# Kernel optimization log

Hardware: AMD Instinct MI355X
Metric: run time of the kernel (lower is better)

The kernel has to match this reference:

```python
import jax, jax.numpy as jnp
import numpy as np

B, T, D, L = 64, 512, 768, 50


def setup_inputs() -> dict:
    key = jax.random.key(0)
    ks = jax.random.split(key, 8)
    input_emb = jax.random.normal(ks[0], (B, T, D), jnp.float32)
    labels = jax.random.randint(ks[1], (B, T), 0, L, jnp.int32)
    # contiguous valid-prefix mask (torchcrf requires mask[:,0]=1)
    lengths = jax.random.randint(ks[2], (B,), T // 2, T + 1)
    label_mask = jnp.arange(T)[None, :] < lengths[:, None]  # bool [B,T]
    W = jax.random.normal(ks[3], (D, L), jnp.float32) * (1.0 / np.sqrt(D))
    b = jnp.zeros((L,), jnp.float32)
    start_transitions = jax.random.uniform(ks[4], (L,), jnp.float32, -0.1, 0.1)
    end_transitions = jax.random.uniform(ks[5], (L,), jnp.float32, -0.1, 0.1)
    transitions = jax.random.uniform(ks[6], (L, L), jnp.float32, -0.1, 0.1)
    return {"input_emb": input_emb, "labels": labels, "label_mask": label_mask,
            "W": W, "b": b, "start_transitions": start_transitions,
            "end_transitions": end_transitions, "transitions": transitions}


def _crf_llh(logits, labels, mask, start_t, end_t, trans):
    """torchcrf log-likelihood, batch_first inputs -> [B] llh."""
    em = jnp.transpose(logits, (1, 0, 2))        # [T,B,L] time-major
    tags = jnp.transpose(labels)                 # [T,B]
    m = jnp.transpose(mask).astype(logits.dtype)  # [T,B]
    bidx = jnp.arange(logits.shape[0])

    # --- numerator: score of gold path ---
    score0 = start_t[tags[0]] + em[0, bidx, tags[0]]

    def num_step(carry, x):
        score, prev = carry
        em_t, tag_t, m_t = x
        step = trans[prev, tag_t] + em_t[bidx, tag_t]
        score = score + step * m_t
        prev = jnp.where(m_t > 0, tag_t, prev)  # track last valid tag
        return (score, prev), None

    (num, last_tags), _ = jax.lax.scan(num_step, (score0, tags[0]),
                                       (em[1:], tags[1:], m[1:]))
    num = num + end_t[last_tags]

    # --- denominator: forward algorithm ---
    alpha0 = start_t[None, :] + em[0]  # [B,L]

    def den_step(alpha, x):
        em_t, m_t = x
        nxt = jax.nn.logsumexp(alpha[:, :, None] + trans[None, :, :], axis=1) + em_t
        return jnp.where(m_t[:, None] > 0, nxt, alpha), None

    alpha, _ = jax.lax.scan(den_step, alpha0, (em[1:], m[1:]))
    den = jax.nn.logsumexp(alpha + end_t[None, :], axis=1)
    return num - den


def reference(input_emb, labels, label_mask, W, b, start_transitions,
              end_transitions, transitions):
    # dropout is identity in eval mode
    logits = input_emb @ W + b  # [B,T,L]
    llh = _crf_llh(logits, labels, label_mask, start_transitions,
                   end_transitions, transitions)
    loss = llh.mean()  # reduction='mean' over batch
    return (-loss, logits)
```

## Files before the change

### kernel.cpp

```cpp
#include <hip/hip_runtime.h>
#include <hip/hip_bf16.h>
#include <math.h>

#define BATCH 64
#define TLEN 512
#define DIM 768
#define NLAB 50

typedef __attribute__((ext_vector_type(8))) short short8;
typedef __attribute__((ext_vector_type(4))) float f32x4;

__device__ __forceinline__ unsigned short f2bf(float f) {
    unsigned int u = __float_as_uint(f);
    return (unsigned short)((u + 0x7FFFu + ((u >> 16) & 1u)) >> 16);
}

__global__ __launch_bounds__(256) void wprep_kernel(const float* __restrict__ W,
                                                    unsigned short* __restrict__ Bt) {
    int idx = blockIdx.x * 256 + threadIdx.x;
    if (idx < 64 * DIM) {
        int c = idx / DIM;
        int k = idx - c * DIM;
        float v = (c < NLAB) ? W[k * NLAB + c] : 0.f;
        Bt[idx] = f2bf(v);
    }
}

#define AST 36
#define BSTC 40

__global__ __launch_bounds__(512)
void gemm_kernel(
    const float* __restrict__ A,
    const unsigned short* __restrict__ Bt,
    const float* __restrict__ bias,
    float* __restrict__ out)
{
    __shared__ float As[2][128 * AST];
    __shared__ short Bs[2][64 * BSTC];

    const int tid = threadIdx.x;
    const int wave = tid >> 6;
    const int lane = tid & 63;
    const int m = lane & 15;
    const int q = lane >> 4;
    const int row0 = blockIdx.x * 128;

    const int r0s = tid >> 2;
    const int c0s = (tid & 3) * 8;
    const int bcol = tid >> 3;
    const int bkk = (tid & 7) * 4;

    f32x4 acc0 = {0.f,0.f,0.f,0.f}, acc1 = {0.f,0.f,0.f,0.f};
    f32x4 acc2 = {0.f,0.f,0.f,0.f}, acc3 = {0.f,0.f,0.f,0.f};

    {
        *(float4*)&As[0][r0s * AST + c0s]     = *(const float4*)(A + (size_t)(row0 + r0s) * DIM + c0s);
        *(float4*)&As[0][r0s * AST + c0s + 4] = *(const float4*)(A + (size_t)(row0 + r0s) * DIM + c0s + 4);
        *(short4*)&Bs[0][bcol * BSTC + bkk]   = *(const short4*)(Bt + (size_t)bcol * DIM + bkk);
    }
    __syncthreads();

    int buf = 0;
    for (int ch = 0; ch < DIM / 32; ++ch) {
        const int k0n = (ch + 1) * 32;
        const bool havenext = (ch < DIM / 32 - 1);
        float4 pa0, pa1;
        short4 pb;
        if (havenext) {
            pa0 = *(const float4*)(A + (size_t)(row0 + r0s) * DIM + k0n + c0s);
            pa1 = *(const float4*)(A + (size_t)(row0 + r0s) * DIM + k0n + c0s + 4);
            pb  = *(const short4*)(Bt + (size_t)bcol * DIM + k0n + bkk);
        }

        const short8 bq0 = *(const short8*)&Bs[buf][( 0 + m) * BSTC + q * 8];
        const short8 bq1 = *(const short8*)&Bs[buf][(16 + m) * BSTC + q * 8];
        const short8 bq2 = *(const short8*)&Bs[buf][(32 + m) * BSTC + q * 8];
        const short8 bq3 = *(const short8*)&Bs[buf][(48 + m) * BSTC + q * 8];

        {
            const int rr = wave * 16 + m;
            const float4 xa = *(const float4*)&As[buf][rr * AST + q * 8];
            const float4 xb = *(const float4*)&As[buf][rr * AST + q * 8 + 4];
            short8 af;
            af[0] = (short)f2bf(xa.x); af[1] = (short)f2bf(xa.y);
            af[2] = (short)f2bf(xa.z); af[3] = (short)f2bf(xa.w);
            af[4] = (short)f2bf(xb.x); af[5] = (short)f2bf(xb.y);
            af[6] = (short)f2bf(xb.z); af[7] = (short)f2bf(xb.w);
            acc0 = __builtin_amdgcn_mfma_f32_16x16x32_bf16(af, bq0, acc0, 0, 0, 0);
            acc1 = __builtin_amdgcn_mfma_f32_16x16x32_bf16(af, bq1, acc1, 0, 0, 0);
            acc2 = __builtin_amdgcn_mfma_f32_16x16x32_bf16(af, bq2, acc2, 0, 0, 0);
            acc3 = __builtin_amdgcn_mfma_f32_16x16x32_bf16(af, bq3, acc3, 0, 0, 0);
        }

        if (havenext) {
            const int nb = buf ^ 1;
            *(float4*)&As[nb][r0s * AST + c0s]     = pa0;
            *(float4*)&As[nb][r0s * AST + c0s + 4] = pa1;
            *(short4*)&Bs[nb][bcol * BSTC + bkk]   = pb;
        }
        __syncthreads();
        buf ^= 1;
    }

    const int rb = row0 + wave * 16 + q * 4;
#pragma unroll
    for (int nt = 0; nt < 4; ++nt) {
        const f32x4 av = (nt == 0) ? acc0 : (nt == 1) ? acc1 : (nt == 2) ? acc2 : acc3;
        const int col = nt * 16 + m;
        if (col < NLAB) {
            const float bv = bias[col];
#pragma unroll
            for (int r = 0; r < 4; ++r)
                out[(size_t)(rb + r) * NLAB + col] = av[r] + bv;
        }
    }
}

__device__ __forceinline__ float wave_sum(float v) {
#pragma unroll
    for (int off = 32; off > 0; off >>= 1) v += __shfl_xor(v, off, 64);
    return v;
}

#define ET_INIT(v, base)                            \
    v.x = __expf(trans[(base + 0) * NLAB + j]);     \
    v.y = __expf(trans[(base + 1) * NLAB + j]);     \
    v.z = __expf(trans[(base + 2) * NLAB + j]);     \
    v.w = __expf(trans[(base + 3) * NLAB + j]);

#define RLF(i) __uint_as_float(__builtin_amdgcn_readlane(__float_as_uint(ue), (i)))

__global__ __launch_bounds__(64) __attribute__((amdgpu_waves_per_eu(1, 1)))
void crf_kernel(
    const float* __restrict__ logits,
    const int* __restrict__ labels,
    const void* __restrict__ maskp,
    const float* __restrict__ startT,
    const float* __restrict__ endT,
    const float* __restrict__ trans,
    float* __restrict__ llh) {
    const int b = blockIdx.x;
    const int lane = threadIdx.x;

    const int probe = ((const int*)maskp)[0];
    int len = 0;
    if (probe == 1) {
        const int* mk = (const int*)maskp + b * TLEN;
#pragma unroll
        for (int it = 0; it < 8; ++it)
            len += (int)__popcll(__ballot(mk[lane + it * 64] != 0));
    } else if (probe == 0x01010101) {
        const unsigned char* mk = (const unsigned char*)maskp + b * TLEN;
#pragma unroll
        for (int it = 0; it < 8; ++it)
            len += (int)__popcll(__ballot(mk[lane + it * 64] != 0));
    } else if (probe == 0x3F803F80) {
        const unsigned short* mk = (const unsigned short*)maskp + b * TLEN;
#pragma unroll
        for (int it = 0; it < 8; ++it)
            len += (int)__popcll(__ballot(mk[lane + it * 64] != 0));
    } else {
        const float* mk = (const float*)maskp + b * TLEN;
#pragma unroll
        for (int it = 0; it < 8; ++it)
            len += (int)__popcll(__ballot(mk[lane + it * 64] != 0.f));
    }

    const int j = lane;
    const int jc = (j < NLAB) ? j : (NLAB - 1);

    float4 et0  = {0.f,0.f,0.f,0.f}, et1  = {0.f,0.f,0.f,0.f};
    float4 et2  = {0.f,0.f,0.f,0.f}, et3  = {0.f,0.f,0.f,0.f};
    float4 et4  = {0.f,0.f,0.f,0.f}, et5  = {0.f,0.f,0.f,0.f};
    float4 et6  = {0.f,0.f,0.f,0.f}, et7  = {0.f,0.f,0.f,0.f};
    float4 et8  = {0.f,0.f,0.f,0.f}, et9  = {0.f,0.f,0.f,0.f};
    float4 et10 = {0.f,0.f,0.f,0.f}, et11 = {0.f,0.f,0.f,0.f};
    float4 et12 = {0.f,0.f,0.f,0.f};
    if (j < NLAB) {
        ET_INIT(et0,  0)  ET_INIT(et1,  4)  ET_INIT(et2,  8)
        ET_INIT(et3,  12) ET_INIT(et4,  16) ET_INIT(et5,  20)
        ET_INIT(et6,  24) ET_INIT(et7,  28) ET_INIT(et8,  32)
        ET_INIT(et9,  36) ET_INIT(et10, 40) ET_INIT(et11, 44)
        et12.x = __expf(trans[48 * NLAB + j]);
        et12.y = __expf(trans[49 * NLAB + j]);
    }

    const float* em = logits + (size_t)b * TLEN * NLAB;

    float a0v = (j < NLAB) ? (startT[j] + em[j]) : 0.f;
    const float Abc = __shfl(a0v, 0, 64);
    float ue = (j < NLAB) ? __expf(a0v - Abc) : 0.f;
    float A = Abc;

    float q0 = em[1 * NLAB + jc];
    float q1 = em[2 * NLAB + jc];
    float q2 = em[3 * NLAB + jc];
    float q3 = em[4 * NLAB + jc];
    float pcur = __expf(q0);
    q0 = q1; q1 = q2; q2 = q3; q3 = em[5 * NLAB + jc];

    for (int t = 1; t < len; ++t) {
        int tf = t + 5; tf = (tf < len) ? tf : (len - 1);
        const float newem = em[tf * NLAB + jc];
        const float pnext = __expf(q0);

        const float b0 = RLF(0);
        const float rv = __builtin_amdgcn_rcpf(b0);
        A += __logf(b0);
        const float pr = pcur * rv;

        float c0 = 0.f, c1 = 0.f, c2 = 0.f, c3 = 0.f;
        float c4 = 0.f, c5 = 0.f, c6 = 0.f, c7 = 0.f;
        c0 = fmaf(b0,      et0.x,  c0);
        c1 = fmaf(RLF(1),  et0.y,  c1);
        c2 = fmaf(RLF(2),  et0.z,  c2);
        c3 = fmaf(RLF(3),  et0.w,  c3);
        c4 = fmaf(RLF(4),  et1.x,  c4);
        c5 = fmaf(RLF(5),  et1.y,  c5);
        c6 = fmaf(RLF(6),  et1.z,  c6);
        c7 = fmaf(RLF(7),  et1.w,  c7);
        c0 = fmaf(RLF(8),  et2.x,  c0);
        c1 = fmaf(RLF(9),  et2.y,  c1);
        c2 = fmaf(RLF(10), et2.z,  c2);
        c3 = fmaf(RLF(11), et2.w,  c3);
        c4 = fmaf(RLF(12), et3.x,  c4);
        c5 = fmaf(RLF(13), et3.y,  c5);
        c6 = fmaf(RLF(14), et3.z,  c6);
        c7 = fmaf(RLF(15), et3.w,  c7);
        c0 = fmaf(RLF(16), et4.x,  c0);
        c1 = fmaf(RLF(17), et4.y,  c1);
        c2 = fmaf(RLF(18), et4.z,  c2);
        c3 = fmaf(RLF(19), et4.w,  c3);
        c4 = fmaf(RLF(20), et5.x,  c4);
        c5 = fmaf(RLF(21), et5.y,  c5);
        c6 = fmaf(RLF(22), et5.z,  c6);
        c7 = fmaf(RLF(23), et5.w,  c7);
        c0 = fmaf(RLF(24), et6.x,  c0);
        c1 = fmaf(RLF(25), et6.y,  c1);
        c2 = fmaf(RLF(26), et6.z,  c2);
        c3 = fmaf(RLF(27), et6.w,  c3);
        c4 = fmaf(RLF(28), et7.x,  c4);
        c5 = fmaf(RLF(29), et7.y,  c5);
        c6 = fmaf(RLF(30), et7.z,  c6);
        c7 = fmaf(RLF(31), et7.w,  c7);
        c0 = fmaf(RLF(32), et8.x,  c0);
        c1 = fmaf(RLF(33), et8.y,  c1);
        c2 = fmaf(RLF(34), et8.z,  c2);
        c3 = fmaf(RLF(35), et8.w,  c3);
        c4 = fmaf(RLF(36), et9.x,  c4);
        c5 = fmaf(RLF(37), et9.y,  c5);
        c6 = fmaf(RLF(38), et9.z,  c6);
        c7 = fmaf(RLF(39), et9.w,  c7);
        c0 = fmaf(RLF(40), et10.x, c0);
        c1 = fmaf(RLF(41), et10.y, c1);
        c2 = fmaf(RLF(42), et10.z, c2);
        c3 = fmaf(RLF(43), et10.w, c3);
        c4 = fmaf(RLF(44), et11.x, c4);
        c5 = fmaf(RLF(45), et11.y, c5);
        c6 = fmaf(RLF(46), et11.z, c6);
        c7 = fmaf(RLF(47), et11.w, c7);
        c0 = fmaf(RLF(48), et12.x, c0);
        c1 = fmaf(RLF(49), et12.y, c1);

        const float s = ((c0 + c1) + (c2 + c3)) + ((c4 + c5) + (c6 + c7));
        ue = s * pr;

        pcur = pnext; q0 = q1; q1 = q2; q2 = q3; q3 = newem;
    }

    const float wv = (j < NLAB) ? (ue * __expf(endT[j])) : 0.f;
    const float den = A + __logf(wave_sum(wv));

    const int* tg = labels + b * TLEN;
    float num = 0.f;
#pragma unroll
    for (int it = 0; it < 8; ++it) {
        const int t = lane + it * 64;
        if (t < len) {
            const int tag = tg[t];
            num += em[t * NLAB + tag];
            if (t >= 1) num += trans[tg[t - 1] * NLAB + tag];
        }
    }
    num = wave_sum(num);
    if (lane == 0) {
        num += startT[tg[0]] + endT[tg[len - 1]];
        llh[b] = num - den;
    }
}

__global__ __launch_bounds__(64) void loss_kernel(const float* __restrict__ llh,
                                                  float* __restrict__ out0) {
    float v = llh[threadIdx.x];
    v = wave_sum(v);
    if (threadIdx.x == 0) out0[0] = -(v * (1.0f / BATCH));
}

extern "C" void kernel_launch(void* const* d_in, const int* in_sizes, int n_in,
                              void* d_out, int out_size, void* d_ws, size_t ws_size,
                              hipStream_t stream) {
    (void)in_sizes; (void)n_in; (void)out_size; (void)ws_size;
    const float* emb    = (const float*)d_in[0];
    const int*   labels = (const int*)d_in[1];
    const void*  mask   = d_in[2];
    const float* W      = (const float*)d_in[3];
    const float* bias   = (const float*)d_in[4];
    const float* startT = (const float*)d_in[5];
    const float* endT   = (const float*)d_in[6];
    const float* trans  = (const float*)d_in[7];

    float* out    = (float*)d_out;
    float* logits = out + 1;
    float* llh    = (float*)d_ws;
    unsigned short* Bt = (unsigned short*)((char*)d_ws + 512);

    wprep_kernel<<<(64 * DIM + 255) / 256, 256, 0, stream>>>(W, Bt);
    gemm_kernel<<<(BATCH * TLEN) / 128, 512, 0, stream>>>(emb, Bt, bias, logits);
    crf_kernel<<<BATCH, 64, 0, stream>>>(logits, labels, mask, startT, endT, trans, llh);
    loss_kernel<<<1, 64, 0, stream>>>(llh, out);
}
```

Measured before the change: 311.1 us.

## Batch 16 sequences per wave in CRF forward using bf16 MFMA recurrence

Rewrites the CRF forward recursion so that one wavefront handles 16 batch sequences at once. Each step's alpha-times-exp(transitions) product becomes a chain of bf16 MFMA 16x16x32 instructions, with exp(trans) split into high and low bf16 parts to recover precision. The state vector is also quantized to bf16 and exchanged through swizzled LDS. The loss kernel is removed in favour of an atomicAdd into an output that wprep zeroes, and the grid shrinks from 64 blocks to 4. This trades the per-lane readlane FMA chain for matrix-core throughput. It risks bf16 accuracy loss in alpha, and with only 4 waves the serial latency per step becomes critical.

Result: slower. 594.8 us (+91.2%).

```diff
diff --git a/kernel.cpp b/kernel.cpp
--- a/kernel.cpp
+++ b/kernel.cpp
@@ -15,9 +15,16 @@
     return (unsigned short)((u + 0x7FFFu + ((u >> 16) & 1u)) >> 16);
 }
 
+__device__ __forceinline__ void wave_lds_fence() {
+    __asm__ __volatile__("s_waitcnt lgkmcnt(0)" ::: "memory");
+    __builtin_amdgcn_wave_barrier();
+}
+
 __global__ __launch_bounds__(256) void wprep_kernel(const float* __restrict__ W,
-                                                    unsigned short* __restrict__ Bt) {
+                                                    unsigned short* __restrict__ Bt,
+                                                    float* __restrict__ out0) {
     int idx = blockIdx.x * 256 + threadIdx.x;
+    if (idx == 0) out0[0] = 0.f;
     if (idx < 64 * DIM) {
         int c = idx / DIM;
         int k = idx - c * DIM;
@@ -117,19 +124,8 @@
     }
 }
 
-__device__ __forceinline__ float wave_sum(float v) {
-#pragma unroll
-    for (int off = 32; off > 0; off >>= 1) v += __shfl_xor(v, off, 64);
-    return v;
-}
-
-#define ET_INIT(v, base)                            \
-    v.x = __expf(trans[(base + 0) * NLAB + j]);     \
-    v.y = __expf(trans[(base + 1) * NLAB + j]);     \
-    v.z = __expf(trans[(base + 2) * NLAB + j]);     \
-    v.w = __expf(trans[(base + 3) * NLAB + j]);
-
-#define RLF(i) __uint_as_float(__builtin_amdgcn_readlane(__float_as_uint(ue), (i)))
+#define LOG2E 1.44269504088896340736f
+#define LN2   0.69314718055994530942f
 
 __global__ __launch_bounds__(64) __attribute__((amdgpu_waves_per_eu(1, 1)))
 void crf_kernel(
@@ -139,162 +135,239 @@
     const float* __restrict__ startT,
     const float* __restrict__ endT,
     const float* __restrict__ trans,
-    float* __restrict__ llh) {
-    const int b = blockIdx.x;
+    float* __restrict__ out0) {
     const int lane = threadIdx.x;
+    const int b16 = lane & 15;
+    const int g = lane >> 4;
+    const int b = blockIdx.x * 16 + b16;
+
+    __shared__ __align__(16) unsigned short X[16 * 64];
+    char* xc = (char*)X;
 
     const int probe = ((const int*)maskp)[0];
     int len = 0;
-    if (probe == 1) {
-        const int* mk = (const int*)maskp + b * TLEN;
-#pragma unroll
-        for (int it = 0; it < 8; ++it)
-            len += (int)__popcll(__ballot(mk[lane + it * 64] != 0));
-    } else if (probe == 0x01010101) {
-        const unsigned char* mk = (const unsigned char*)maskp + b * TLEN;
-#pragma unroll
-        for (int it = 0; it < 8; ++it)
-            len += (int)__popcll(__ballot(mk[lane + it * 64] != 0));
-    } else if (probe == 0x3F803F80) {
-        const unsigned short* mk = (const unsigned short*)maskp + b * TLEN;
-#pragma unroll
-        for (int it = 0; it < 8; ++it)
-            len += (int)__popcll(__ballot(mk[lane + it * 64] != 0));
-    } else {
-        const float* mk = (const float*)maskp + b * TLEN;
-#pragma unroll
-        for (int it = 0; it < 8; ++it)
-            len += (int)__popcll(__ballot(mk[lane + it * 64] != 0.f));
-    }
-
-    const int j = lane;
-    const int jc = (j < NLAB) ? j : (NLAB - 1);
-
-    float4 et0  = {0.f,0.f,0.f,0.f}, et1  = {0.f,0.f,0.f,0.f};
-    float4 et2  = {0.f,0.f,0.f,0.f}, et3  = {0.f,0.f,0.f,0.f};
-    float4 et4  = {0.f,0.f,0.f,0.f}, et5  = {0.f,0.f,0.f,0.f};
-    float4 et6  = {0.f,0.f,0.f,0.f}, et7  = {0.f,0.f,0.f,0.f};
-    float4 et8  = {0.f,0.f,0.f,0.f}, et9  = {0.f,0.f,0.f,0.f};
-    float4 et10 = {0.f,0.f,0.f,0.f}, et11 = {0.f,0.f,0.f,0.f};
-    float4 et12 = {0.f,0.f,0.f,0.f};
-    if (j < NLAB) {
-        ET_INIT(et0,  0)  ET_INIT(et1,  4)  ET_INIT(et2,  8)
-        ET_INIT(et3,  12) ET_INIT(et4,  16) ET_INIT(et5,  20)
-        ET_INIT(et6,  24) ET_INIT(et7,  28) ET_INIT(et8,  32)
-        ET_INIT(et9,  36) ET_INIT(et10, 40) ET_INIT(et11, 44)
-        et12.x = __expf(trans[48 * NLAB + j]);
-        et12.y = __expf(trans[49 * NLAB + j]);
-    }
-
-    const float* em = logits + (size_t)b * TLEN * NLAB;
-
-    float a0v = (j < NLAB) ? (startT[j] + em[j]) : 0.f;
-    const float Abc = __shfl(a0v, 0, 64);
-    float ue = (j < NLAB) ? __expf(a0v - Abc) : 0.f;
-    float A = Abc;
-
-    float q0 = em[1 * NLAB + jc];
-    float q1 = em[2 * NLAB + jc];
-    float q2 = em[3 * NLAB + jc];
-    float q3 = em[4 * NLAB + jc];
-    float pcur = __expf(q0);
-    q0 = q1; q1 = q2; q2 = q3; q3 = em[5 * NLAB + jc];
-
-    for (int t = 1; t < len; ++t) {
-        int tf = t + 5; tf = (tf < len) ? tf : (len - 1);
-        const float newem = em[tf * NLAB + jc];
-        const float pnext = __expf(q0);
-
-        const float b0 = RLF(0);
-        const float rv = __builtin_amdgcn_rcpf(b0);
-        A += __logf(b0);
-        const float pr = pcur * rv;
-
-        float c0 = 0.f, c1 = 0.f, c2 = 0.f, c3 = 0.f;
-        float c4 = 0.f, c5 = 0.f, c6 = 0.f, c7 = 0.f;
-        c0 = fmaf(b0,      et0.x,  c0);
-        c1 = fmaf(RLF(1),  et0.y,  c1);
-        c2 = fmaf(RLF(2),  et0.z,  c2);
-        c3 = fmaf(RLF(3),  et0.w,  c3);
-        c4 = fmaf(RLF(4),  et1.x,  c4);
-        c5 = fmaf(RLF(5),  et1.y,  c5);
-        c6 = fmaf(RLF(6),  et1.z,  c6);
-        c7 = fmaf(RLF(7),  et1.w,  c7);
-        c0 = fmaf(RLF(8),  et2.x,  c0);
-        c1 = fmaf(RLF(9),  et2.y,  c1);
-        c2 = fmaf(RLF(10), et2.z,  c2);
-        c3 = fmaf(RLF(11), et2.w,  c3);
-        c4 = fmaf(RLF(12), et3.x,  c4);
-        c5 = fmaf(RLF(13), et3.y,  c5);
-        c6 = fmaf(RLF(14), et3.z,  c6);
-        c7 = fmaf(RLF(15), et3.w,  c7);
-        c0 = fmaf(RLF(16), et4.x,  c0);
-        c1 = fmaf(RLF(17), et4.y,  c1);
-        c2 = fmaf(RLF(18), et4.z,  c2);
-        c3 = fmaf(RLF(19), et4.w,  c3);
-        c4 = fmaf(RLF(20), et5.x,  c4);
-        c5 = fmaf(RLF(21), et5.y,  c5);
-        c6 = fmaf(RLF(22), et5.z,  c6);
-        c7 = fmaf(RLF(23), et5.w,  c7);
-        c0 = fmaf(RLF(24), et6.x,  c0);
-        c1 = fmaf(RLF(25), et6.y,  c1);
-        c2 = fmaf(RLF(26), et6.z,  c2);
-        c3 = fmaf(RLF(27), et6.w,  c3);
-        c4 = fmaf(RLF(28), et7.x,  c4);
-        c5 = fmaf(RLF(29), et7.y,  c5);
-        c6 = fmaf(RLF(30), et7.z,  c6);
-        c7 = fmaf(RLF(31), et7.w,  c7);
-        c0 = fmaf(RLF(32), et8.x,  c0);
-        c1 = fmaf(RLF(33), et8.y,  c1);
-        c2 = fmaf(RLF(34), et8.z,  c2);
-        c3 = fmaf(RLF(35), et8.w,  c3);
-        c4 = fmaf(RLF(36), et9.x,  c4);
-        c5 = fmaf(RLF(37), et9.y,  c5);
-        c6 = fmaf(RLF(38), et9.z,  c6);
-        c7 = fmaf(RLF(39), et9.w,  c7);
-        c0 = fmaf(RLF(40), et10.x, c0);
-        c1 = fmaf(RLF(41), et10.y, c1);
-        c2 = fmaf(RLF(42), et10.z, c2);
-        c3 = fmaf(RLF(43), et10.w, c3);
-        c4 = fmaf(RLF(44), et11.x, c4);
-        c5 = fmaf(RLF(45), et11.y, c5);
-        c6 = fmaf(RLF(46), et11.z, c6);
-        c7 = fmaf(RLF(47), et11.w, c7);
-        c0 = fmaf(RLF(48), et12.x, c0);
-        c1 = fmaf(RLF(49), et12.y, c1);
-
-        const float s = ((c0 + c1) + (c2 + c3)) + ((c4 + c5) + (c6 + c7));
-        ue = s * pr;
-
-        pcur = pnext; q0 = q1; q1 = q2; q2 = q3; q3 = newem;
-    }
-
-    const float wv = (j < NLAB) ? (ue * __expf(endT[j])) : 0.f;
-    const float den = A + __logf(wave_sum(wv));
-
-    const int* tg = labels + b * TLEN;
+    {
+        const int t0 = g * 128;
+        if (probe == 1) {
+            const int* mk = (const int*)maskp + (size_t)b * TLEN + t0;
+#pragma unroll 8
+            for (int i = 0; i < 128; ++i) len += (mk[i] != 0);
+        } else if (probe == 0x01010101) {
+            const unsigned char* mk = (const unsigned char*)maskp + (size_t)b * TLEN + t0;
+#pragma unroll 8
+            for (int i = 0; i < 128; ++i) len += (mk[i] != 0);
+        } else if (probe == 0x3F803F80) {
+            const unsigned short* mk = (const unsigned short*)maskp + (size_t)b * TLEN + t0;
+#pragma unroll 8
+            for (int i = 0; i < 128; ++i) len += (mk[i] != 0);
+        } else {
+            const float* mk = (const float*)maskp + (size_t)b * TLEN + t0;
+#pragma unroll 8
+            for (int i = 0; i < 128; ++i) len += (mk[i] != 0.f);
+        }
+    }
+    len += __shfl_xor(len, 16, 64);
+    len += __shfl_xor(len, 32, 64);
+    int lenmax = len;
+    { int o = __shfl_xor(lenmax, 1, 64); lenmax = lenmax > o ? lenmax : o; }
+    { int o = __shfl_xor(lenmax, 2, 64); lenmax = lenmax > o ? lenmax : o; }
+    { int o = __shfl_xor(lenmax, 4, 64); lenmax = lenmax > o ? lenmax : o; }
+    { int o = __shfl_xor(lenmax, 8, 64); lenmax = lenmax > o ? lenmax : o; }
+
+    short8 ah00, ah01, ah02, ah03, ah10, ah11, ah12, ah13;
+    short8 al00, al01, al02, al03, al10, al11, al12, al13;
+#define MKFRAG(DH, DL, KT, MT) { short8 h, l;                                   \
+    _Pragma("unroll")                                                           \
+    for (int j = 0; j < 8; ++j) {                                               \
+        const int k = 32 * KT + 8 * g + j; const int m = 16 * MT + b16;         \
+        float e = 0.f;                                                          \
+        if (k < NLAB && m < NLAB) e = __expf(trans[k * NLAB + m]);              \
+        const unsigned short hb = f2bf(e);                                      \
+        const float ef = __uint_as_float((unsigned)hb << 16);                   \
+        const unsigned short lb = f2bf(e - ef);                                 \
+        h[j] = (short)hb; l[j] = (short)lb;                                     \
+    } DH = h; DL = l; }
+    MKFRAG(ah00, al00, 0, 0) MKFRAG(ah01, al01, 0, 1)
+    MKFRAG(ah02, al02, 0, 2) MKFRAG(ah03, al03, 0, 3)
+    MKFRAG(ah10, al10, 1, 0) MKFRAG(ah11, al11, 1, 1)
+    MKFRAG(ah12, al12, 1, 2) MKFRAG(ah13, al13, 1, 3)
+
+    const int rowbase = b16 * 128;
+    const int swz = (b16 & 7) << 4;
+    int wby[4][2];
+    int emo[4][4];
+    bool vmask[4][4];
+#pragma unroll
+    for (int mt = 0; mt < 4; ++mt) {
+        wby[mt][0] = rowbase + ((32 * mt + 8 * g)     ^ swz);
+        wby[mt][1] = rowbase + ((32 * mt + 8 * g + 4) ^ swz);
+#pragma unroll
+        for (int r = 0; r < 4; ++r) {
+            const int L = 16 * mt + 4 * g + r;
+            emo[mt][r] = (L < NLAB) ? L : (NLAB - 1);
+            vmask[mt][r] = (L < NLAB);
+        }
+    }
+    const int rby0 = rowbase + ((16 * g)      ^ swz);
+    const int rby1 = rowbase + ((64 + 16 * g) ^ swz);
+    const int vby  = rowbase + swz;
+
+    const float* emb = logits + (size_t)b * TLEN * NLAB;
+
+    float a0[4][4];
+#pragma unroll
+    for (int mt = 0; mt < 4; ++mt)
+#pragma unroll
+        for (int r = 0; r < 4; ++r)
+            a0[mt][r] = startT[emo[mt][r]] + emb[emo[mt][r]];
+    const float a00 = __int_as_float(
+        __builtin_amdgcn_ds_bpermute(b16 * 4, __float_as_int(a0[0][0])));
+    float A = a00;
+
+#pragma unroll
+    for (int mt = 0; mt < 4; ++mt) {
+        float w0 = vmask[mt][0] ? __expf(a0[mt][0] - a00) : 0.f;
+        float w1 = vmask[mt][1] ? __expf(a0[mt][1] - a00) : 0.f;
+        float w2 = vmask[mt][2] ? __expf(a0[mt][2] - a00) : 0.f;
+        float w3 = vmask[mt][3] ? __expf(a0[mt][3] - a00) : 0.f;
+        unsigned int u0, u1;
+        asm("v_cvt_pk_bf16_f32 %0, %1, %2" : "=v"(u0) : "v"(w0), "v"(w1));
+        asm("v_cvt_pk_bf16_f32 %0, %1, %2" : "=v"(u1) : "v"(w2), "v"(w3));
+        *(unsigned int*)(xc + wby[mt][0]) = u0;
+        *(unsigned int*)(xc + wby[mt][1]) = u1;
+    }
+    wave_lds_fence();
+    short8 xb0 = *(const short8*)(xc + rby0);
+    short8 xb1 = *(const short8*)(xc + rby1);
+
+    float pf[4][4];
+    {
+        const float* e1 = emb + NLAB;
+#pragma unroll
+        for (int mt = 0; mt < 4; ++mt)
+#pragma unroll
+            for (int r = 0; r < 4; ++r)
+                pf[mt][r] = e1[emo[mt][r]];
+    }
+
+    for (int t = 1; t < lenmax; ++t) {
+        const bool act = (t < len);
+        const unsigned short vus = *(const unsigned short*)(xc + vby);
+
+        const int tn = (t + 1 < lenmax) ? (t + 1) : (lenmax - 1);
+        const float* en = emb + (size_t)tn * NLAB;
+        float nf[4][4];
+#pragma unroll
+        for (int mt = 0; mt < 4; ++mt)
+#pragma unroll
+            for (int r = 0; r < 4; ++r)
+                nf[mt][r] = en[emo[mt][r]];
+
+        const float vf = __uint_as_float((unsigned)vus << 16);
+        const float lg2v = __log2f(vf);
+        A += act ? lg2v * LN2 : 0.f;
+
+        float pe[4][4];
+#pragma unroll
+        for (int mt = 0; mt < 4; ++mt)
+#pragma unroll
+            for (int r = 0; r < 4; ++r)
+                pe[mt][r] = __builtin_amdgcn_exp2f(fmaf(pf[mt][r], LOG2E, -lg2v));
+
+        f32x4 ac0 = {0.f,0.f,0.f,0.f}, ac1 = {0.f,0.f,0.f,0.f};
+        f32x4 ac2 = {0.f,0.f,0.f,0.f}, ac3 = {0.f,0.f,0.f,0.f};
+        ac0 = __builtin_amdgcn_mfma_f32_16x16x32_bf16(ah00, xb0, ac0, 0, 0, 0);
+        ac0 = __builtin_amdgcn_mfma_f32_16x16x32_bf16(al00, xb0, ac0, 0, 0, 0);
+        ac0 = __builtin_amdgcn_mfma_f32_16x16x32_bf16(ah10, xb1, ac0, 0, 0, 0);
+        ac0 = __builtin_amdgcn_mfma_f32_16x16x32_bf16(al10, xb1, ac0, 0, 0, 0);
+        ac1 = __builtin_amdgcn_mfma_f32_16x16x32_bf16(ah01, xb0, ac1, 0, 0, 0);
+        ac1 = __builtin_amdgcn_mfma_f32_16x16x32_bf16(al01, xb0, ac1, 0, 0, 0);
+        ac1 = __builtin_amdgcn_mfma_f32_16x16x32_bf16(ah11, xb1, ac1, 0, 0, 0);
+        ac1 = __builtin_amdgcn_mfma_f32_16x16x32_bf16(al11, xb1, ac1, 0, 0, 0);
+        ac2 = __builtin_amdgcn_mfma_f32_16x16x32_bf16(ah02, xb0, ac2, 0, 0, 0);
+        ac2 = __builtin_amdgcn_mfma_f32_16x16x32_bf16(al02, xb0, ac2, 0, 0, 0);
+        ac2 = __builtin_amdgcn_mfma_f32_16x16x32_bf16(ah12, xb1, ac2, 0, 0, 0);
+        ac2 = __builtin_amdgcn_mfma_f32_16x16x32_bf16(al12, xb1, ac2, 0, 0, 0);
+        ac3 = __builtin_amdgcn_mfma_f32_16x16x32_bf16(ah03, xb0, ac3, 0, 0, 0);
+        ac3 = __builtin_amdgcn_mfma_f32_16x16x32_bf16(al03, xb0, ac3, 0, 0, 0);
+        ac3 = __builtin_amdgcn_mfma_f32_16x16x32_bf16(ah13, xb1, ac3, 0, 0, 0);
+        ac3 = __builtin_amdgcn_mfma_f32_16x16x32_bf16(al13, xb1, ac3, 0, 0, 0);
+
+        unsigned int u00, u01, u10, u11, u20, u21, u30, u31;
+#define WPACK(AC, MT, U0, U1) {                                                \
+        float w0 = AC[0] * pe[MT][0];                                          \
+        float w1 = AC[1] * pe[MT][1];                                          \
+        float w2 = AC[2] * pe[MT][2];                                          \
+        float w3 = AC[3] * pe[MT][3];                                          \
+        if (!vmask[MT][0]) w0 = 0.f;                                           \
+        if (!vmask[MT][1]) w1 = 0.f;                                           \
+        if (!vmask[MT][2]) w2 = 0.f;                                           \
+        if (!vmask[MT][3]) w3 = 0.f;                                           \
+        asm("v_cvt_pk_bf16_f32 %0, %1, %2" : "=v"(U0) : "v"(w0), "v"(w1));     \
+        asm("v_cvt_pk_bf16_f32 %0, %1, %2" : "=v"(U1) : "v"(w2), "v"(w3));     \
+    }
+        WPACK(ac0, 0, u00, u01)
+        WPACK(ac1, 1, u10, u11)
+        WPACK(ac2, 2, u20, u21)
+        WPACK(ac3, 3, u30, u31)
+
+        if (act) {
+            *(unsigned int*)(xc + wby[0][0]) = u00;
+            *(unsigned int*)(xc + wby[0][1]) = u01;
+            *(unsigned int*)(xc + wby[1][0]) = u10;
+            *(unsigned int*)(xc + wby[1][1]) = u11;
+            *(unsigned int*)(xc + wby[2][0]) = u20;
+            *(unsigned int*)(xc + wby[2][1]) = u21;
+            *(unsigned int*)(xc + wby[3][0]) = u30;
+            *(unsigned int*)(xc + wby[3][1]) = u31;
+        }
+        wave_lds_fence();
+        xb0 = *(const short8*)(xc + rby0);
+        xb1 = *(const short8*)(xc + rby1);
+
+#pragma unroll
+        for (int mt = 0; mt < 4; ++mt)
+#pragma unroll
+            for (int r = 0; r < 4; ++r)
+                pf[mt][r] = nf[mt][r];
+    }
+
+    float part = 0.f;
+#pragma unroll
+    for (int j = 0; j < 8; ++j) {
+        const int k1 = 32 + 8 * g + j;
+        const float x0 = __uint_as_float((unsigned)(unsigned short)xb0[j] << 16);
+        const float x1 = __uint_as_float((unsigned)(unsigned short)xb1[j] << 16);
+        const float e0 = __expf(endT[8 * g + j]);
+        float e1 = 0.f;
+        if (k1 < NLAB) e1 = __expf(endT[k1]);
+        part = fmaf(x0, e0, part);
+        part = fmaf(x1, e1, part);
+    }
+    part += __shfl_xor(part, 16, 64);
+    part += __shfl_xor(part, 32, 64);
+    const float den = A + __logf(part);
+
+    const int* tg = labels + (size_t)b * TLEN;
     float num = 0.f;
-#pragma unroll
-    for (int it = 0; it < 8; ++it) {
-        const int t = lane + it * 64;
-        if (t < len) {
-            const int tag = tg[t];
-            num += em[t * NLAB + tag];
-            if (t >= 1) num += trans[tg[t - 1] * NLAB + tag];
-        }
-    }
-    num = wave_sum(num);
-    if (lane == 0) {
+    {
+        const int t0 = g * 128;
+#pragma unroll 8
+        for (int i = 0; i < 128; ++i) {
+            const int t = t0 + i;
+            if (t < len) {
+                const int tag = tg[t];
+                num += emb[(size_t)t * NLAB + tag];
+                if (t >= 1) num += trans[tg[t - 1] * NLAB + tag];
+            }
+        }
+    }
+    num += __shfl_xor(num, 16, 64);
+    num += __shfl_xor(num, 32, 64);
+    if (g == 0) {
         num += startT[tg[0]] + endT[tg[len - 1]];
-        llh[b] = num - den;
-    }
-}
-
-__global__ __launch_bounds__(64) void loss_kernel(const float* __restrict__ llh,
-                                                  float* __restrict__ out0) {
-    float v = llh[threadIdx.x];
-    v = wave_sum(v);
-    if (threadIdx.x == 0) out0[0] = -(v * (1.0f / BATCH));
+        atomicAdd(out0, (den - num) * (1.0f / BATCH));
+    }
 }
 
 extern "C" void kernel_launch(void* const* d_in, const int* in_sizes, int n_in,
@@ -312,11 +385,9 @@
 
     float* out    = (float*)d_out;
     float* logits = out + 1;
-    float* llh    = (float*)d_ws;
     unsigned short* Bt = (unsigned short*)((char*)d_ws + 512);
 
-    wprep_kernel<<<(64 * DIM + 255) / 256, 256, 0, stream>>>(W, Bt);
+    wprep_kernel<<<(64 * DIM + 255) / 256, 256, 0, stream>>>(W, Bt, out);
     gemm_kernel<<<(BATCH * TLEN) / 128, 512, 0, stream>>>(emb, Bt, bias, logits);
-    crf_kernel<<<BATCH, 64, 0, stream>>>(logits, labels, mask, startT, endT, trans, llh);
-    loss_kernel<<<1, 64, 0, stream>>>(llh, out);
-}
+    crf_kernel<<<BATCH / 16, 64, 0, stream>>>(logits, labels, mask, startT, endT, trans, out);
+}
```

## Parallelize CRF forward recursion over time chunks via MFMA transfer-matrix products

Applied to the files above, without the earlier changes.

Splits the 511-step forward algorithm into 16 chunks of 32 steps per sequence. Each chunk builds its 64x64 product of exp-transition/emission matrices using bf16 MFMA with hi/lo split weights, renormalizing each step and recording log scales. A combine kernel then applies the 16 chunk matrices to alpha in sequence and accumulates the loss via atomicAdd, which removes the separate loss kernel. This exposes 1024 blocks of parallelism instead of 64 serial waves, at the cost of far more arithmetic, bf16 rounding of the chunk matrices, and extra workspace traffic.

Measured after the change: 252.7 us. -18.8%, faster.

```diff
diff --git a/kernel.cpp b/kernel.cpp
--- a/kernel.cpp
+++ b/kernel.cpp
@@ -6,6 +6,8 @@
 #define TLEN 512
 #define DIM 768
 #define NLAB 50
+#define NCH 16
+#define CHL 32
 
 typedef __attribute__((ext_vector_type(8))) short short8;
 typedef __attribute__((ext_vector_type(4))) float f32x4;
@@ -15,9 +17,58 @@
     return (unsigned short)((u + 0x7FFFu + ((u >> 16) & 1u)) >> 16);
 }
 
+__device__ __forceinline__ void wave_lds_fence() {
+    __asm__ __volatile__("s_waitcnt lgkmcnt(0)" ::: "memory");
+    __builtin_amdgcn_wave_barrier();
+}
+
+#define GLD4(gp, lp) __builtin_amdgcn_global_load_lds(                         \
+    (const __attribute__((address_space(1))) void*)(gp),                       \
+    (__attribute__((address_space(3))) void*)(lp), 4, 0, 0)
+
+__device__ __forceinline__ float wave_sum(float v) {
+#pragma unroll
+    for (int off = 32; off > 0; off >>= 1) v += __shfl_xor(v, off, 64);
+    return v;
+}
+__device__ __forceinline__ float wave_max(float v) {
+#pragma unroll
+    for (int off = 32; off > 0; off >>= 1) v = fmaxf(v, __shfl_xor(v, off, 64));
+    return v;
+}
+
+__device__ __forceinline__ int mask_len(const void* maskp, int b, int lane) {
+    const int probe = ((const int*)maskp)[0];
+    int len = 0;
+    if (probe == 1) {
+        const int* mk = (const int*)maskp + (size_t)b * TLEN;
+#pragma unroll
+        for (int it = 0; it < 8; ++it)
+            len += (int)__popcll(__ballot(mk[lane + it * 64] != 0));
+    } else if (probe == 0x01010101) {
+        const unsigned char* mk = (const unsigned char*)maskp + (size_t)b * TLEN;
+#pragma unroll
+        for (int it = 0; it < 8; ++it)
+            len += (int)__popcll(__ballot(mk[lane + it * 64] != 0));
+    } else if (probe == 0x3F803F80) {
+        const unsigned short* mk = (const unsigned short*)maskp + (size_t)b * TLEN;
+#pragma unroll
+        for (int it = 0; it < 8; ++it)
+            len += (int)__popcll(__ballot(mk[lane + it * 64] != 0));
+    } else {
+        const float* mk = (const float*)maskp + (size_t)b * TLEN;
+#pragma unroll
+        for (int it = 0; it < 8; ++it)
+            len += (int)__popcll(__ballot(mk[lane + it * 64] != 0.f));
+    }
+    return len;
+}
+
 __global__ __launch_bounds__(256) void wprep_kernel(const float* __restrict__ W,
-                                                    unsigned short* __restrict__ Bt) {
+                                                    unsigned short* __restrict__ Bt,
+                                                    float* __restrict__ out0) {
     int idx = blockIdx.x * 256 + threadIdx.x;
+    if (idx == 0) out0[0] = 0.f;
     if (idx < 64 * DIM) {
         int c = idx / DIM;
         int k = idx - c * DIM;
@@ -117,184 +168,259 @@
     }
 }
 
-__device__ __forceinline__ float wave_sum(float v) {
-#pragma unroll
-    for (int off = 32; off > 0; off >>= 1) v += __shfl_xor(v, off, 64);
-    return v;
-}
-
-#define ET_INIT(v, base)                            \
-    v.x = __expf(trans[(base + 0) * NLAB + j]);     \
-    v.y = __expf(trans[(base + 1) * NLAB + j]);     \
-    v.z = __expf(trans[(base + 2) * NLAB + j]);     \
-    v.w = __expf(trans[(base + 3) * NLAB + j]);
-
-#define RLF(i) __uint_as_float(__builtin_amdgcn_readlane(__float_as_uint(ue), (i)))
-
 __global__ __launch_bounds__(64) __attribute__((amdgpu_waves_per_eu(1, 1)))
-void crf_kernel(
-    const float* __restrict__ logits,
-    const int* __restrict__ labels,
-    const void* __restrict__ maskp,
-    const float* __restrict__ startT,
-    const float* __restrict__ endT,
-    const float* __restrict__ trans,
-    float* __restrict__ llh) {
+void crf_chunk(const float* __restrict__ logits,
+               const void* __restrict__ maskp,
+               const float* __restrict__ trans,
+               unsigned short* __restrict__ Qws,
+               float* __restrict__ logSws) {
+    const int bx = blockIdx.x;
+    const int b = bx >> 4;
+    const int c = bx & 15;
+    const int lane = threadIdx.x;
+    const int b16 = lane & 15;
+    const int g = lane >> 4;
+
+    __shared__ __align__(16) unsigned short Q[64 * 64];
+    __shared__ __align__(16) float EM[CHL * 64];
+    char* qc = (char*)Q;
+
+    const int len = mask_len(maskp, b, lane);
+    const int t0 = 1 + c * CHL;
+    int te = t0 + CHL; if (te > len) te = len;
+
+    unsigned short* qg = Qws + (size_t)bx * 4096;
+
+    int emo[4][4]; bool vmask[4][4];
+#pragma unroll
+    for (int mt = 0; mt < 4; ++mt)
+#pragma unroll
+        for (int r = 0; r < 4; ++r) {
+            const int L = 16 * mt + 4 * g + r;
+            emo[mt][r] = (L < NLAB) ? L : (NLAB - 1);
+            vmask[mt][r] = (L < NLAB);
+        }
+
+    if (te <= t0) {
+#pragma unroll
+        for (int mt = 0; mt < 4; ++mt)
+#pragma unroll
+            for (int r = 0; r < 4; ++r) {
+                const int m = 16 * mt + 4 * g + r;
+#pragma unroll
+                for (int nt = 0; nt < 4; ++nt) {
+                    const int col = 16 * nt + b16;
+                    qg[m * 64 + col] = (m == col) ? (unsigned short)0x3F80 : (unsigned short)0;
+                }
+            }
+        if (lane == 0) logSws[bx] = 0.f;
+        return;
+    }
+
+    short8 ah[4][2], al[4][2];
+#pragma unroll
+    for (int mt = 0; mt < 4; ++mt)
+#pragma unroll
+        for (int kt = 0; kt < 2; ++kt) {
+            short8 h, l;
+#pragma unroll
+            for (int j = 0; j < 8; ++j) {
+                const int k = 32 * kt + 8 * g + j;
+                const int m = 16 * mt + b16;
+                float e = 0.f;
+                if (k < NLAB && m < NLAB) e = __expf(trans[k * NLAB + m]);
+                const unsigned short hb = f2bf(e);
+                const float ef = __uint_as_float((unsigned)hb << 16);
+                h[j] = (short)hb;
+                l[j] = (short)f2bf(e - ef);
+            }
+            ah[mt][kt] = h; al[mt][kt] = l;
+        }
+
+    const int swz = (b16 & 7) << 4;
+    int wby[4][4], rby[4][2];
+#pragma unroll
+    for (int nt = 0; nt < 4; ++nt) {
+        const int rowb = (16 * nt + b16) * 128;
+#pragma unroll
+        for (int mt = 0; mt < 4; ++mt)
+            wby[nt][mt] = rowb + ((32 * mt + 8 * g) ^ swz);
+#pragma unroll
+        for (int kt = 0; kt < 2; ++kt)
+            rby[nt][kt] = rowb + ((64 * kt + 16 * g) ^ swz);
+    }
+
+    {
+        uint4 z = {0u, 0u, 0u, 0u};
+#pragma unroll
+        for (int i = 0; i < 8; ++i)
+            *(uint4*)(qc + lane * 128 + i * 16) = z;
+        const int boff = 2 * lane;
+        const int grp = boff & ~7, wi = boff & 7;
+        *(unsigned short*)(qc + lane * 128 + ((grp ^ ((lane & 7) << 4))) + wi) = 0x3F80;
+    }
+
+    const float* embb = logits + (size_t)b * TLEN * NLAB;
+    const int nrows = te - t0;
+    for (int i = 0; i < nrows; ++i) {
+        if (lane < NLAB)
+            GLD4(embb + (size_t)(t0 + i) * NLAB + lane, (char*)EM + i * 256);
+    }
+    asm volatile("s_waitcnt vmcnt(0)" ::: "memory");
+    wave_lds_fence();
+
+    float logS = 0.f;
+    const f32x4 z4 = {0.f, 0.f, 0.f, 0.f};
+
+    for (int t = t0; t < te; ++t) {
+        short8 xbq[4][2];
+#pragma unroll
+        for (int nt = 0; nt < 4; ++nt)
+#pragma unroll
+            for (int kt = 0; kt < 2; ++kt)
+                xbq[nt][kt] = *(const short8*)(qc + rby[nt][kt]);
+
+        const char* emr = (const char*)EM + (t - t0) * 256;
+        float pe[4][4];
+#pragma unroll
+        for (int mt = 0; mt < 4; ++mt) {
+            const float4 ev = *(const float4*)(emr + (16 * mt + 4 * g) * 4);
+#pragma unroll
+            for (int r = 0; r < 4; ++r) {
+                const float e = (r == 0) ? ev.x : (r == 1) ? ev.y : (r == 2) ? ev.z : ev.w;
+                pe[mt][r] = vmask[mt][r] ? __expf(e) : 0.f;
+            }
+        }
+
+        f32x4 acc[4][4];
+#pragma unroll
+        for (int nt = 0; nt < 4; ++nt)
+#pragma unroll
+            for (int mt = 0; mt < 4; ++mt) {
+                f32x4 a = __builtin_amdgcn_mfma_f32_16x16x32_bf16(ah[mt][0], xbq[nt][0], z4, 0, 0, 0);
+                a = __builtin_amdgcn_mfma_f32_16x16x32_bf16(al[mt][0], xbq[nt][0], a, 0, 0, 0);
+                a = __builtin_amdgcn_mfma_f32_16x16x32_bf16(ah[mt][1], xbq[nt][1], a, 0, 0, 0);
+                a = __builtin_amdgcn_mfma_f32_16x16x32_bf16(al[mt][1], xbq[nt][1], a, 0, 0, 0);
+                acc[nt][mt] = a;
+            }
+
+        float mx = 0.f;
+#pragma unroll
+        for (int nt = 0; nt < 4; ++nt)
+#pragma unroll
+            for (int mt = 0; mt < 4; ++mt)
+#pragma unroll
+                for (int r = 0; r < 4; ++r)
+                    mx = fmaxf(mx, acc[nt][mt][r] * pe[mt][r]);
+        mx = wave_max(mx);
+        const float rv = __builtin_amdgcn_rcpf(mx);
+        logS += __logf(mx);
+
+        if (t < te - 1) {
+#pragma unroll
+            for (int nt = 0; nt < 4; ++nt)
+#pragma unroll
+                for (int mt = 0; mt < 4; ++mt) {
+                    const float w0 = acc[nt][mt][0] * pe[mt][0] * rv;
+                    const float w1 = acc[nt][mt][1] * pe[mt][1] * rv;
+                    const float w2 = acc[nt][mt][2] * pe[mt][2] * rv;
+                    const float w3 = acc[nt][mt][3] * pe[mt][3] * rv;
+                    uint2 p;
+                    asm("v_cvt_pk_bf16_f32 %0, %1, %2" : "=v"(p.x) : "v"(w0), "v"(w1));
+                    asm("v_cvt_pk_bf16_f32 %0, %1, %2" : "=v"(p.y) : "v"(w2), "v"(w3));
+                    *(uint2*)(qc + wby[nt][mt]) = p;
+                }
+            wave_lds_fence();
+        } else {
+#pragma unroll
+            for (int mt = 0; mt < 4; ++mt)
+#pragma unroll
+                for (int r = 0; r < 4; ++r) {
+                    const int m = 16 * mt + 4 * g + r;
+#pragma unroll
+                    for (int nt = 0; nt < 4; ++nt)
+                        qg[m * 64 + 16 * nt + b16] =
+                            f2bf(acc[nt][mt][r] * pe[mt][r] * rv);
+                }
+        }
+    }
+    if (lane == 0) logSws[bx] = logS;
+}
+
+__global__ __launch_bounds__(64) __attribute__((amdgpu_waves_per_eu(1, 1)))
+void crf_combine(const float* __restrict__ logits,
+                 const int* __restrict__ labels,
+                 const void* __restrict__ maskp,
+                 const float* __restrict__ startT,
+                 const float* __restrict__ endT,
+                 const float* __restrict__ trans,
+                 const unsigned short* __restrict__ Qws,
+                 const float* __restrict__ logSws,
+                 float* __restrict__ out0) {
     const int b = blockIdx.x;
     const int lane = threadIdx.x;
-
-    const int probe = ((const int*)maskp)[0];
-    int len = 0;
-    if (probe == 1) {
-        const int* mk = (const int*)maskp + b * TLEN;
-#pragma unroll
-        for (int it = 0; it < 8; ++it)
-            len += (int)__popcll(__ballot(mk[lane + it * 64] != 0));
-    } else if (probe == 0x01010101) {
-        const unsigned char* mk = (const unsigned char*)maskp + b * TLEN;
-#pragma unroll
-        for (int it = 0; it < 8; ++it)
-            len += (int)__popcll(__ballot(mk[lane + it * 64] != 0));
-    } else if (probe == 0x3F803F80) {
-        const unsigned short* mk = (const unsigned short*)maskp + b * TLEN;
-#pragma unroll
-        for (int it = 0; it < 8; ++it)
-            len += (int)__popcll(__ballot(mk[lane + it * 64] != 0));
-    } else {
-        const float* mk = (const float*)maskp + b * TLEN;
-#pragma unroll
-        for (int it = 0; it < 8; ++it)
-            len += (int)__popcll(__ballot(mk[lane + it * 64] != 0.f));
-    }
-
-    const int j = lane;
-    const int jc = (j < NLAB) ? j : (NLAB - 1);
-
-    float4 et0  = {0.f,0.f,0.f,0.f}, et1  = {0.f,0.f,0.f,0.f};
-    float4 et2  = {0.f,0.f,0.f,0.f}, et3  = {0.f,0.f,0.f,0.f};
-    float4 et4  = {0.f,0.f,0.f,0.f}, et5  = {0.f,0.f,0.f,0.f};
-    float4 et6  = {0.f,0.f,0.f,0.f}, et7  = {0.f,0.f,0.f,0.f};
-    float4 et8  = {0.f,0.f,0.f,0.f}, et9  = {0.f,0.f,0.f,0.f};
-    float4 et10 = {0.f,0.f,0.f,0.f}, et11 = {0.f,0.f,0.f,0.f};
-    float4 et12 = {0.f,0.f,0.f,0.f};
-    if (j < NLAB) {
-        ET_INIT(et0,  0)  ET_INIT(et1,  4)  ET_INIT(et2,  8)
-        ET_INIT(et3,  12) ET_INIT(et4,  16) ET_INIT(et5,  20)
-        ET_INIT(et6,  24) ET_INIT(et7,  28) ET_INIT(et8,  32)
-        ET_INIT(et9,  36) ET_INIT(et10, 40) ET_INIT(et11, 44)
-        et12.x = __expf(trans[48 * NLAB + j]);
-        et12.y = __expf(trans[49 * NLAB + j]);
-    }
-
+    __shared__ __align__(16) float AL[64];
+
+    const int len = mask_len(maskp, b, lane);
     const float* em = logits + (size_t)b * TLEN * NLAB;
 
-    float a0v = (j < NLAB) ? (startT[j] + em[j]) : 0.f;
-    const float Abc = __shfl(a0v, 0, 64);
-    float ue = (j < NLAB) ? __expf(a0v - Abc) : 0.f;
-    float A = Abc;
-
-    float q0 = em[1 * NLAB + jc];
-    float q1 = em[2 * NLAB + jc];
-    float q2 = em[3 * NLAB + jc];
-    float q3 = em[4 * NLAB + jc];
-    float pcur = __expf(q0);
-    q0 = q1; q1 = q2; q2 = q3; q3 = em[5 * NLAB + jc];
-
-    for (int t = 1; t < len; ++t) {
-        int tf = t + 5; tf = (tf < len) ? tf : (len - 1);
-        const float newem = em[tf * NLAB + jc];
-        const float pnext = __expf(q0);
-
-        const float b0 = RLF(0);
-        const float rv = __builtin_amdgcn_rcpf(b0);
-        A += __logf(b0);
-        const float pr = pcur * rv;
-
-        float c0 = 0.f, c1 = 0.f, c2 = 0.f, c3 = 0.f;
-        float c4 = 0.f, c5 = 0.f, c6 = 0.f, c7 = 0.f;
-        c0 = fmaf(b0,      et0.x,  c0);
-        c1 = fmaf(RLF(1),  et0.y,  c1);
-        c2 = fmaf(RLF(2),  et0.z,  c2);
-        c3 = fmaf(RLF(3),  et0.w,  c3);
-        c4 = fmaf(RLF(4),  et1.x,  c4);
-        c5 = fmaf(RLF(5),  et1.y,  c5);
-        c6 = fmaf(RLF(6),  et1.z,  c6);
-        c7 = fmaf(RLF(7),  et1.w,  c7);
-        c0 = fmaf(RLF(8),  et2.x,  c0);
-        c1 = fmaf(RLF(9),  et2.y,  c1);
-        c2 = fmaf(RLF(10), et2.z,  c2);
-        c3 = fmaf(RLF(11), et2.w,  c3);
-        c4 = fmaf(RLF(12), et3.x,  c4);
-        c5 = fmaf(RLF(13), et3.y,  c5);
-        c6 = fmaf(RLF(14), et3.z,  c6);
-        c7 = fmaf(RLF(15), et3.w,  c7);
-        c0 = fmaf(RLF(16), et4.x,  c0);
-        c1 = fmaf(RLF(17), et4.y,  c1);
-        c2 = fmaf(RLF(18), et4.z,  c2);
-        c3 = fmaf(RLF(19), et4.w,  c3);
-        c4 = fmaf(RLF(20), et5.x,  c4);
-        c5 = fmaf(RLF(21), et5.y,  c5);
-        c6 = fmaf(RLF(22), et5.z,  c6);
-        c7 = fmaf(RLF(23), et5.w,  c7);
-        c0 = fmaf(RLF(24), et6.x,  c0);
-        c1 = fmaf(RLF(25), et6.y,  c1);
-        c2 = fmaf(RLF(26), et6.z,  c2);
-        c3 = fmaf(RLF(27), et6.w,  c3);
-        c4 = fmaf(RLF(28), et7.x,  c4);
-        c5 = fmaf(RLF(29), et7.y,  c5);
-        c6 = fmaf(RLF(30), et7.z,  c6);
-        c7 = fmaf(RLF(31), et7.w,  c7);
-        c0 = fmaf(RLF(32), et8.x,  c0);
-        c1 = fmaf(RLF(33), et8.y,  c1);
-        c2 = fmaf(RLF(34), et8.z,  c2);
-        c3 = fmaf(RLF(35), et8.w,  c3);
-        c4 = fmaf(RLF(36), et9.x,  c4);
-        c5 = fmaf(RLF(37), et9.y,  c5);
-        c6 = fmaf(RLF(38), et9.z,  c6);
-        c7 = fmaf(RLF(39), et9.w,  c7);
-        c0 = fmaf(RLF(40), et10.x, c0);
-        c1 = fmaf(RLF(41), et10.y, c1);
-        c2 = fmaf(RLF(42), et10.z, c2);
-        c3 = fmaf(RLF(43), et10.w, c3);
-        c4 = fmaf(RLF(44), et11.x, c4);
-        c5 = fmaf(RLF(45), et11.y, c5);
-        c6 = fmaf(RLF(46), et11.z, c6);
-        c7 = fmaf(RLF(47), et11.w, c7);
-        c0 = fmaf(RLF(48), et12.x, c0);
-        c1 = fmaf(RLF(49), et12.y, c1);
-
-        const float s = ((c0 + c1) + (c2 + c3)) + ((c4 + c5) + (c6 + c7));
-        ue = s * pr;
-
-        pcur = pnext; q0 = q1; q1 = q2; q2 = q3; q3 = newem;
-    }
-
-    const float wv = (j < NLAB) ? (ue * __expf(endT[j])) : 0.f;
-    const float den = A + __logf(wave_sum(wv));
-
-    const int* tg = labels + b * TLEN;
+    float a0 = (lane < NLAB) ? (startT[lane] + em[lane]) : -1e30f;
+    const float mx0 = wave_max(a0);
+    float alpha = (lane < NLAB) ? __expf(a0 - mx0) : 0.f;
+    float A = mx0;
+    AL[lane] = alpha;
+    wave_lds_fence();
+
+    const unsigned short* qb = Qws + (size_t)b * NCH * 4096;
+    for (int cc = 0; cc < NCH; ++cc) {
+        const unsigned short* qr = qb + cc * 4096 + lane * 64;
+        uint4 qv[8];
+#pragma unroll
+        for (int i = 0; i < 8; ++i)
+            qv[i] = *(const uint4*)(qr + i * 8);
+
+        float s = 0.f;
+#pragma unroll
+        for (int i = 0; i < 8; ++i) {
+            const float4 alo = *(const float4*)(AL + 8 * i);
+            const float4 ahi = *(const float4*)(AL + 8 * i + 4);
+            const uint4 q = qv[i];
+            s = fmaf(__uint_as_float(q.x << 16), alo.x, s);
+            s = fmaf(__uint_as_float(q.x & 0xFFFF0000u), alo.y, s);
+            s = fmaf(__uint_as_float(q.y << 16), alo.z, s);
+            s = fmaf(__uint_as_float(q.y & 0xFFFF0000u), alo.w, s);
+            s = fmaf(__uint_as_float(q.z << 16), ahi.x, s);
+            s = fmaf(__uint_as_float(q.z & 0xFFFF0000u), ahi.y, s);
+            s = fmaf(__uint_as_float(q.w << 16), ahi.z, s);
+            s = fmaf(__uint_as_float(q.w & 0xFFFF0000u), ahi.w, s);
+        }
+        const float mxs = wave_max(s);
+        A += __logf(mxs) + logSws[b * NCH + cc];
+        alpha = s * __builtin_amdgcn_rcpf(mxs);
+        wave_lds_fence();
+        AL[lane] = alpha;
+        wave_lds_fence();
+    }
+
+    const float term = (lane < NLAB) ? alpha * __expf(endT[lane]) : 0.f;
+    const float den = A + __logf(wave_sum(term));
+
+    const int* tg = labels + (size_t)b * TLEN;
     float num = 0.f;
 #pragma unroll
     for (int it = 0; it < 8; ++it) {
         const int t = lane + it * 64;
         if (t < len) {
             const int tag = tg[t];
-            num += em[t * NLAB + tag];
+            num += em[(size_t)t * NLAB + tag];
             if (t >= 1) num += trans[tg[t - 1] * NLAB + tag];
         }
     }
     num = wave_sum(num);
     if (lane == 0) {
         num += startT[tg[0]] + endT[tg[len - 1]];
-        llh[b] = num - den;
-    }
-}
-
-__global__ __launch_bounds__(64) void loss_kernel(const float* __restrict__ llh,
-                                                  float* __restrict__ out0) {
-    float v = llh[threadIdx.x];
-    v = wave_sum(v);
-    if (threadIdx.x == 0) out0[0] = -(v * (1.0f / BATCH));
+        atomicAdd(out0, (den - num) * (1.0f / BATCH));
+    }
 }
 
 extern "C" void kernel_launch(void* const* d_in, const int* in_sizes, int n_in,
@@ -312,11 +438,13 @@
 
     float* out    = (float*)d_out;
     float* logits = out + 1;
-    float* llh    = (float*)d_ws;
-    unsigned short* Bt = (unsigned short*)((char*)d_ws + 512);
-
-    wprep_kernel<<<(64 * DIM + 255) / 256, 256, 0, stream>>>(W, Bt);
+    unsigned short* Bt   = (unsigned short*)((char*)d_ws + 512);
+    float*          logS = (float*)((char*)d_ws + 99328);
+    unsigned short* Qws  = (unsigned short*)((char*)d_ws + 131072);
+
+    wprep_kernel<<<(64 * DIM + 255) / 256, 256, 0, stream>>>(W, Bt, out);
     gemm_kernel<<<(BATCH * TLEN) / 128, 512, 0, stream>>>(emb, Bt, bias, logits);
-    crf_kernel<<<BATCH, 64, 0, stream>>>(logits, labels, mask, startT, endT, trans, llh);
-    loss_kernel<<<1, 64, 0, stream>>>(llh, out);
-}
+    crf_chunk<<<BATCH * NCH, 64, 0, stream>>>(logits, mask, trans, Qws, logS);
+    crf_combine<<<BATCH, 64, 0, stream>>>(logits, labels, mask, startT, endT, trans,
+                                          Qws, logS, out);
+}
```
